# Performance work log

Measured on AMD Instinct MI355X. Metric: run time of the kernel, lower is better.

The kernel has to match this reference:

```python
import jax, jax.numpy as jnp
import numpy as np

B = 262144      # parallel environments / batch
N_IN = 4        # sensory neurons (hardcoded n_inputs=4 in TWC)
N_HID = 64      # hidden interneurons
N_OUT = 8       # output/motor neurons
N_EDGES = 128   # sparse gap-junction edges in->hid
STEPS = 4       # internal_steps


def setup_inputs() -> dict:
    key = jax.random.key(0)
    ks = jax.random.split(key, 18)
    rn = lambda k, s, sc=1.0: jax.random.normal(k, s, dtype=jnp.float32) * sc
    return {
        'x':           rn(ks[0], (B, N_IN)),
        'hid_E0':      rn(ks[1], (B, N_HID), 0.1),
        'hid_O0':      rn(ks[2], (B, N_HID), 0.1),
        'out_E0':      rn(ks[3], (B, N_OUT), 0.1),
        'out_O0':      rn(ks[4], (B, N_OUT), 0.1),
        'w_in2hid_IN': rn(ks[5], (N_IN, N_HID), 0.1),
        'w_hid_IN':    rn(ks[6], (N_HID, N_HID), 0.1),
        'w_hid_EX':    rn(ks[7], (N_HID, N_HID), 0.1),
        'w_hid2out':   rn(ks[8], (N_HID, N_OUT), 0.1),
        'gj_w':        rn(ks[9], (N_EDGES,), 0.1),
        'th_in':       rn(ks[10], (N_IN,), 0.1),
        'dec_in':      jax.random.uniform(ks[11], (N_IN,), dtype=jnp.float32),
        'th_hid':      rn(ks[12], (N_HID,), 0.1),
        'dec_hid':     jax.random.uniform(ks[13], (N_HID,), dtype=jnp.float32),
        'th_out':      rn(ks[14], (N_OUT,), 0.1),
        'dec_out':     jax.random.uniform(ks[15], (N_OUT,), dtype=jnp.float32),
        'gj_src':      jax.random.randint(ks[16], (N_EDGES,), 0, N_IN, dtype=jnp.int32),
        'gj_dst':      jax.random.randint(ks[17], (N_EDGES,), 0, N_HID, dtype=jnp.int32),
    }


def _gate(E, th):
    # FIURI neuron output: pass internal state when above threshold, else 0
    return jnp.where(E >= th, E, jnp.zeros_like(E))


def reference(x, hid_E0, hid_O0, out_E0, out_O0,
              w_in2hid_IN, w_hid_IN, w_hid_EX, w_hid2out, gj_w,
              th_in, dec_in, th_hid, dec_hid, th_out, dec_out,
              gj_src, gj_dst):
    sp = jax.nn.softplus
    # obs encoder: ex_in + in_in == x (passthrough split into +/- parts)
    o_in_pre = x                              # in_O used for all connections
    # input layer neuron_step on state (x, x): leak only, no external input
    E_in = dec_in * x                         # [B, N_IN]
    O_in = _gate(E_in, th_in)

    # loop-invariant dense influences (TWC uses the ORIGINAL hid O each iter)
    in2hid = -(o_in_pre @ sp(w_in2hid_IN))    # inhibitory dense conn [B,N_HID]
    hid2hid = hid_O0 @ (sp(w_hid_EX) - sp(w_hid_IN))  # EX + IN dense conns
    # sparse gap junction: I_gj[b,j] = sum_e sp(gj_w[e])*(o_pre[b,src]-E[b,dst])
    sw = sp(gj_w)
    M = jnp.zeros((N_IN, N_HID), x.dtype).at[gj_src, gj_dst].add(sw)
    deg = jnp.zeros((N_HID,), x.dtype).at[gj_dst].add(sw)
    gj_in = o_in_pre @ M                      # [B, N_HID], loop-invariant part
    I_const = in2hid + hid2hid + gj_in

    E_hid, O_hid = hid_E0, hid_O0
    for _ in range(STEPS):
        E_hid = dec_hid * E_hid + I_const - deg * E_hid
        O_hid = _gate(E_hid, th_hid)

    # output layer driven by the ORIGINAL hid O (per TWC._recurrent_step)
    h2o = hid_O0 @ sp(w_hid2out)              # excitatory dense conn [B,N_OUT]
    E_out = dec_out * out_E0 + h2o
    O_out = _gate(E_out, th_out)
    action = jnp.tanh(E_out)                  # action_decoder on internal E
    return (action, E_in, O_in, E_hid, O_hid, E_out, O_out)
```

## Files before the change

kernel.cpp:

```cpp
#include <hip/hip_runtime.h>
#include <math.h>

#define NT 256
#define RPB 64

typedef __attribute__((ext_vector_type(8))) short bf16x8;
typedef __attribute__((ext_vector_type(4))) float f32x4;

__device__ __forceinline__ float softplus_f(float v) {
    return fmaxf(v, 0.0f) + log1pf(expf(-fabsf(v)));
}
__device__ __forceinline__ unsigned short bfr(float f) {
    unsigned int u = __float_as_uint(f);
    u += 0x7FFFu + ((u >> 16) & 1u);
    return (unsigned short)(u >> 16);
}
__device__ __forceinline__ unsigned int bfpack(float a, float b) {
    return (unsigned int)bfr(a) | ((unsigned int)bfr(b) << 16);
}


__global__ __launch_bounds__(NT) void twc_prep(
    const float* __restrict__ w_in2hid,
    const float* __restrict__ w_hid_IN,
    const float* __restrict__ w_hid_EX,
    const float* __restrict__ w_hid2out,
    const float* __restrict__ gj_w,
    const float* __restrict__ th_in,
    const float* __restrict__ dec_in,
    const float* __restrict__ th_hid,
    const float* __restrict__ dec_hid,
    const float* __restrict__ th_out,
    const float* __restrict__ dec_out,
    const int* __restrict__ gj_src,
    const int* __restrict__ gj_dst,
    float* __restrict__ ws)
{
    const int t = threadIdx.x;
    const int blk = blockIdx.x;
    unsigned short* wsS = (unsigned short*)ws;
    if (blk < 30) {
        const int e = blk * NT + t;
        const int col = e / 96, k = e - col * 96;
        if (col < 64 && k >= 64 && k < 68) return;
        float v = 0.0f;
        if (col < 64 && k < 64)
            v = softplus_f(w_hid_EX[k * 64 + col]) - softplus_f(w_hid_IN[k * 64 + col]);
        else if (col >= 64 && col < 72 && k < 64)
            v = softplus_f(w_hid2out[k * 8 + (col - 64)]);
        wsS[e] = bfr(v);
    } else {
        __shared__ float sw[128];
        __shared__ int ssrc[128], sdst[128];
        if (t < 128) { sw[t] = softplus_f(gj_w[t]); ssrc[t] = gj_src[t]; sdst[t] = gj_dst[t]; }
        __syncthreads();
        if (t < 64) {
            const int j = t;
            float m0 = 0.f, m1 = 0.f, m2 = 0.f, m3 = 0.f, deg = 0.f;
            #pragma unroll 4
            for (int e = 0; e < 128; ++e) {
                const float w = (sdst[e] == j) ? sw[e] : 0.0f;
                deg += w;
                const int se = ssrc[e];
                m0 += (se == 0) ? w : 0.0f;
                m1 += (se == 1) ? w : 0.0f;
                m2 += (se == 2) ? w : 0.0f;
                m3 += (se == 3) ? w : 0.0f;
            }
            wsS[j * 96 + 64] = bfr(m0 - softplus_f(w_in2hid[0 * 64 + j]));
            wsS[j * 96 + 65] = bfr(m1 - softplus_f(w_in2hid[1 * 64 + j]));
            wsS[j * 96 + 66] = bfr(m2 - softplus_f(w_in2hid[2 * 64 + j]));
            wsS[j * 96 + 67] = bfr(m3 - softplus_f(w_in2hid[3 * 64 + j]));
            const float a  = dec_hid[j] - deg;
            const float a2 = a * a;
            ws[3840 + j] = a2 * a2;
            ws[3904 + j] = 1.0f + a + a2 + a2 * a;
            ws[3968 + j] = th_hid[j];
        }
        if (t < 4) { ws[4032 + t] = dec_in[t];  ws[4036 + t] = th_in[t]; }
        if (t < 8) { ws[4040 + t] = dec_out[t]; ws[4048 + t] = th_out[t]; }
    }
}

__global__ __launch_bounds__(NT, 4) void twc_main(
    const float* __restrict__ x,
    const float* __restrict__ hidE0,
    const float* __restrict__ hidO0,
    const float* __restrict__ outE0,
    const float* __restrict__ ws,
    float* __restrict__ out, int B)
{
    __shared__ __align__(16) unsigned int slds[8704];
    const int t = threadIdx.x;
    const size_t rowBase = (size_t)blockIdx.x * RPB;
    const size_t Bs = (size_t)B;
    float4* out4 = (float4*)out;
    const float* wsf = ws;

    float4 e0pre[4];
    float eo0pre[2];
    {
        const float4* gE0 = (const float4*)hidE0 + rowBase * 16;
        #pragma unroll
        for (int j = 0; j < 4; ++j) e0pre[j] = gE0[j * NT + t];
        #pragma unroll
        for (int j = 0; j < 2; ++j) eo0pre[j] = outE0[rowBase * 8 + j * NT + t];
    }

    {
        const float4* wsv = (const float4*)ws;
        float4* l4 = (float4*)slds;
        #pragma unroll
        for (int j = 0; j < 4; ++j) {
            const int i = j * NT + t;
            if (i < 960) l4[i] = wsv[i];
        }
    }
    {
        const float4* gO0 = (const float4*)hidO0 + rowBase * 16;
        #pragma unroll
        for (int j = 0; j < 4; ++j) {
            const int i = j * NT + t;
            const float4 v = gO0[i];
            const int row = i >> 4, c4 = i & 15;
            const int base = 3840 + row * 48 + c4 * 2;
            slds[base]     = bfpack(v.x, v.y);
            slds[base + 1] = bfpack(v.z, v.w);
        }
        #pragma unroll
        for (int j = 0; j < 2; ++j) {
            const int i = j * NT + t;
            if (i < 448) {
                const int row = i / 7, p = i - row * 7;
                const int base = 3840 + row * 48 + 34 + p * 2;
                slds[base] = 0u; slds[base + 1] = 0u;
            }
        }
        if (t < 64) {
            const float4 xv = ((const float4*)x)[rowBase + t];
            const int base = 3840 + t * 48 + 32;
            slds[base]     = bfpack(xv.x, xv.y);
            slds[base + 1] = bfpack(xv.z, xv.w);
            const float4 di = ((const float4*)ws)[1008];
            const float4 ti = ((const float4*)ws)[1009];
            float4 Ein, Oin;
            Ein.x = di.x * xv.x; Ein.y = di.y * xv.y; Ein.z = di.z * xv.z; Ein.w = di.w * xv.w;
            Oin.x = (Ein.x >= ti.x) ? Ein.x : 0.0f;
            Oin.y = (Ein.y >= ti.y) ? Ein.y : 0.0f;
            Oin.z = (Ein.z >= ti.z) ? Ein.z : 0.0f;
            Oin.w = (Ein.w >= ti.w) ? Ein.w : 0.0f;
            out4[Bs * 2 + rowBase + t] = Ein;
            out4[Bs * 3 + rowBase + t] = Oin;
        }
    }
    __syncthreads();

    const int l = t & 63, w = t >> 6;
    const int fr = l & 15, lg = l >> 4;
    f32x4 acc[5];
    {
        const f32x4 z = {0.0f, 0.0f, 0.0f, 0.0f};
        #pragma unroll
        for (int ct = 0; ct < 5; ++ct) acc[ct] = z;
        const short* Ash = (const short*)(slds + 3840) + (w * 16 + fr) * 96 + lg * 8;
        const short* Bsh = (const short*)slds + fr * 96 + lg * 8;
        #pragma unroll
        for (int s = 0; s < 3; ++s) {
            const bf16x8 af = *(const bf16x8*)(Ash + s * 32);
            #pragma unroll
            for (int ct = 0; ct < 5; ++ct) {
                const bf16x8 bv = *(const bf16x8*)(Bsh + ct * 1536 + s * 32);
                acc[ct] = __builtin_amdgcn_mfma_f32_16x16x32_bf16(af, bv, acc[ct], 0, 0, 0);
            }
        }
    }
    __syncthreads();

    {
        float* buf = (float*)(slds + 3840);
        const int rowl = w * 16 + lg * 4;
        #pragma unroll
        for (int ct = 0; ct < 4; ++ct) {
            const int c = ct * 16 + fr;
            const float qs = wsf[3904 + c];
            #pragma unroll
            for (int r = 0; r < 4; ++r)
                buf[(rowl + r) * 76 + c] = qs * acc[ct][r];
        }
        if (fr < 8) {
            #pragma unroll
            for (int r = 0; r < 4; ++r)
                buf[(rowl + r) * 76 + 64 + fr] = acc[4][r];
        }
    }
    __syncthreads();

    {
        const float* buf = (const float*)(slds + 3840);
        const float4* th4 = (const float4*)ws + 992;
        const float4* p44 = (const float4*)ws + 960;
        #pragma unroll
        for (int j = 0; j < 4; ++j) {
            const int i = j * NT + t;
            const int row = i >> 4, c4 = i & 15;
            const float4 qi = *(const float4*)&buf[row * 76 + c4 * 4];
            const float4 p4 = p44[c4];
            const float4 e0 = e0pre[j];
            const float4 th = th4[c4];
            float4 E, O;
            E.x = fmaf(p4.x, e0.x, qi.x);
            E.y = fmaf(p4.y, e0.y, qi.y);
            E.z = fmaf(p4.z, e0.z, qi.z);
            E.w = fmaf(p4.w, e0.w, qi.w);
            O.x = (E.x >= th.x) ? E.x : 0.0f;
            O.y = (E.y >= th.y) ? E.y : 0.0f;
            O.z = (E.z >= th.z) ? E.z : 0.0f;
            O.w = (E.w >= th.w) ? E.w : 0.0f;
            out4[Bs * 4  + rowBase * 16 + i] = E;
            out4[Bs * 20 + rowBase * 16 + i] = O;
        }
        #pragma unroll
        for (int j = 0; j < 2; ++j) {
            const int idx = j * NT + t;
            const int row = idx >> 3, q = idx & 7;
            const float h  = buf[row * 76 + 64 + q];
            const float eo = fmaf(wsf[4040 + q], eo0pre[j], h);
            out[rowBase * 8 + idx]            = tanhf(eo);
            out[Bs * 144 + rowBase * 8 + idx] = eo;
            out[Bs * 152 + rowBase * 8 + idx] = (eo >= wsf[4048 + q]) ? eo : 0.0f;
        }
    }
}

extern "C" void kernel_launch(void* const* d_in, const int* in_sizes, int n_in,
                              void* d_out, int out_size, void* d_ws, size_t ws_size,
                              hipStream_t stream) {
    (void)n_in; (void)out_size; (void)ws_size;
    const float* x        = (const float*)d_in[0];
    const float* hidE0    = (const float*)d_in[1];
    const float* hidO0    = (const float*)d_in[2];
    const float* outE0    = (const float*)d_in[3];
    const float* w_in2hid = (const float*)d_in[5];
    const float* w_hid_IN = (const float*)d_in[6];
    const float* w_hid_EX = (const float*)d_in[7];
    const float* w_hid2out= (const float*)d_in[8];
    const float* gj_w     = (const float*)d_in[9];
    const float* th_in    = (const float*)d_in[10];
    const float* dec_in   = (const float*)d_in[11];
    const float* th_hid   = (const float*)d_in[12];
    const float* dec_hid  = (const float*)d_in[13];
    const float* th_out   = (const float*)d_in[14];
    const float* dec_out  = (const float*)d_in[15];
    const int*   gj_src   = (const int*)d_in[16];
    const int*   gj_dst   = (const int*)d_in[17];
    float* out = (float*)d_out;
    float* ws  = (float*)d_ws;

    const int B = in_sizes[0] / 4;

    twc_prep<<<31, NT, 0, stream>>>(
        w_in2hid, w_hid_IN, w_hid_EX, w_hid2out, gj_w,
        th_in, dec_in, th_hid, dec_hid, th_out, dec_out,
        gj_src, gj_dst, ws);

    twc_main<<<B / RPB, NT, 0, stream>>>(x, hidE0, hidO0, outE0, ws, out, B);
}
```

Before: 80.12 us.

## Load MFMA operands directly from global memory, skipping LDS staging

After: 82.37 us. 1.03x slower.

```diff
diff --git a/kernel.cpp b/kernel.cpp
--- a/kernel.cpp
+++ b/kernel.cpp
@@ -90,8 +90,10 @@
     const float* __restrict__ ws,
     float* __restrict__ out, int B)
 {
-    __shared__ __align__(16) unsigned int slds[8704];
+    __shared__ __align__(16) float buf[64 * 76];
     const int t = threadIdx.x;
+    const int l = t & 63, w = t >> 6;
+    const int fr = l & 15, lg = l >> 4;
     const size_t rowBase = (size_t)blockIdx.x * RPB;
     const size_t Bs = (size_t)B;
     float4* out4 = (float4*)out;
@@ -107,77 +109,57 @@
         for (int j = 0; j < 2; ++j) eo0pre[j] = outE0[rowBase * 8 + j * NT + t];
     }
 
-    {
-        const float4* wsv = (const float4*)ws;
-        float4* l4 = (float4*)slds;
-        #pragma unroll
-        for (int j = 0; j < 4; ++j) {
-            const int i = j * NT + t;
-            if (i < 960) l4[i] = wsv[i];
-        }
-    }
-    {
-        const float4* gO0 = (const float4*)hidO0 + rowBase * 16;
-        #pragma unroll
-        for (int j = 0; j < 4; ++j) {
-            const int i = j * NT + t;
-            const float4 v = gO0[i];
-            const int row = i >> 4, c4 = i & 15;
-            const int base = 3840 + row * 48 + c4 * 2;
-            slds[base]     = bfpack(v.x, v.y);
-            slds[base + 1] = bfpack(v.z, v.w);
-        }
-        #pragma unroll
-        for (int j = 0; j < 2; ++j) {
-            const int i = j * NT + t;
-            if (i < 448) {
-                const int row = i / 7, p = i - row * 7;
-                const int base = 3840 + row * 48 + 34 + p * 2;
-                slds[base] = 0u; slds[base + 1] = 0u;
-            }
-        }
-        if (t < 64) {
-            const float4 xv = ((const float4*)x)[rowBase + t];
-            const int base = 3840 + t * 48 + 32;
-            slds[base]     = bfpack(xv.x, xv.y);
-            slds[base + 1] = bfpack(xv.z, xv.w);
-            const float4 di = ((const float4*)ws)[1008];
-            const float4 ti = ((const float4*)ws)[1009];
-            float4 Ein, Oin;
-            Ein.x = di.x * xv.x; Ein.y = di.y * xv.y; Ein.z = di.z * xv.z; Ein.w = di.w * xv.w;
-            Oin.x = (Ein.x >= ti.x) ? Ein.x : 0.0f;
-            Oin.y = (Ein.y >= ti.y) ? Ein.y : 0.0f;
-            Oin.z = (Ein.z >= ti.z) ? Ein.z : 0.0f;
-            Oin.w = (Ein.w >= ti.w) ? Ein.w : 0.0f;
-            out4[Bs * 2 + rowBase + t] = Ein;
-            out4[Bs * 3 + rowBase + t] = Oin;
-        }
-    }
-    __syncthreads();
-
-    const int l = t & 63, w = t >> 6;
-    const int fr = l & 15, lg = l >> 4;
+    const int arow = w * 16 + fr;
+    bf16x8 af0, af1, af2;
+    {
+        const float4* gO0r = (const float4*)hidO0 + (rowBase + arow) * 16;
+        const float4 v0 = gO0r[lg * 2],     v1 = gO0r[lg * 2 + 1];
+        const float4 v2 = gO0r[8 + lg * 2], v3 = gO0r[8 + lg * 2 + 1];
+        unsigned int a0[4] = { bfpack(v0.x, v0.y), bfpack(v0.z, v0.w),
+                               bfpack(v1.x, v1.y), bfpack(v1.z, v1.w) };
+        unsigned int a1[4] = { bfpack(v2.x, v2.y), bfpack(v2.z, v2.w),
+                               bfpack(v3.x, v3.y), bfpack(v3.z, v3.w) };
+        af0 = *(const bf16x8*)a0;
+        af1 = *(const bf16x8*)a1;
+        unsigned int a2[4] = { 0u, 0u, 0u, 0u };
+        if (lg == 0) {
+            const float4 xr = ((const float4*)x)[rowBase + arow];
+            a2[0] = bfpack(xr.x, xr.y);
+            a2[1] = bfpack(xr.z, xr.w);
+        }
+        af2 = *(const bf16x8*)a2;
+    }
+
+    if (t < 64) {
+        const float4 xv = ((const float4*)x)[rowBase + t];
+        const float4 di = ((const float4*)ws)[1008];
+        const float4 ti = ((const float4*)ws)[1009];
+        float4 Ein, Oin;
+        Ein.x = di.x * xv.x; Ein.y = di.y * xv.y; Ein.z = di.z * xv.z; Ein.w = di.w * xv.w;
+        Oin.x = (Ein.x >= ti.x) ? Ein.x : 0.0f;
+        Oin.y = (Ein.y >= ti.y) ? Ein.y : 0.0f;
+        Oin.z = (Ein.z >= ti.z) ? Ein.z : 0.0f;
+        Oin.w = (Ein.w >= ti.w) ? Ein.w : 0.0f;
+        out4[Bs * 2 + rowBase + t] = Ein;
+        out4[Bs * 3 + rowBase + t] = Oin;
+    }
+
     f32x4 acc[5];
     {
         const f32x4 z = {0.0f, 0.0f, 0.0f, 0.0f};
         #pragma unroll
         for (int ct = 0; ct < 5; ++ct) acc[ct] = z;
-        const short* Ash = (const short*)(slds + 3840) + (w * 16 + fr) * 96 + lg * 8;
-        const short* Bsh = (const short*)slds + fr * 96 + lg * 8;
-        #pragma unroll
-        for (int s = 0; s < 3; ++s) {
-            const bf16x8 af = *(const bf16x8*)(Ash + s * 32);
-            #pragma unroll
-            for (int ct = 0; ct < 5; ++ct) {
-                const bf16x8 bv = *(const bf16x8*)(Bsh + ct * 1536 + s * 32);
-                acc[ct] = __builtin_amdgcn_mfma_f32_16x16x32_bf16(af, bv, acc[ct], 0, 0, 0);
-            }
-        }
-    }
-    __syncthreads();
-
-    {
-        float* buf = (float*)(slds + 3840);
+        const bf16x8* wsB = (const bf16x8*)ws;
+        #pragma unroll
+        for (int ct = 0; ct < 5; ++ct) {
+            const int cb = (ct * 16 + fr) * 12 + lg;
+            acc[ct] = __builtin_amdgcn_mfma_f32_16x16x32_bf16(af0, wsB[cb],     acc[ct], 0, 0, 0);
+            acc[ct] = __builtin_amdgcn_mfma_f32_16x16x32_bf16(af1, wsB[cb + 4], acc[ct], 0, 0, 0);
+            acc[ct] = __builtin_amdgcn_mfma_f32_16x16x32_bf16(af2, wsB[cb + 8], acc[ct], 0, 0, 0);
+        }
+    }
+
+    {
         const int rowl = w * 16 + lg * 4;
         #pragma unroll
         for (int ct = 0; ct < 4; ++ct) {
@@ -196,7 +178,6 @@
     __syncthreads();
 
     {
-        const float* buf = (const float*)(slds + 3840);
         const float4* th4 = (const float4*)ws + 992;
         const float4* p44 = (const float4*)ws + 960;
         #pragma unroll
```
